# Kernel optimization log

Measured on AMD Instinct MI355X. Metric: run time of the kernel, lower is better.

Reference implementation:

```python
import jax, jax.numpy as jnp
import numpy as np

POOLED = 7          # output_size (7x7 bins)
SPATIAL_SCALE = 0.0625  # 1/16 backbone stride


def setup_inputs() -> dict:
    key = jax.random.key(0)
    k1, k2, k3, k4 = jax.random.split(key, 4)
    B, C, H, W = 4, 1029, 80, 80   # C = output_dim(21) * 7 * 7
    N = 1024                        # number of ROIs
    x = jax.random.normal(k1, (B, C, H, W), dtype=jnp.float32)
    img_w = W / SPATIAL_SCALE       # 1280 px
    img_h = H / SPATIAL_SCALE
    bidx = jax.random.randint(k2, (N,), 0, B).astype(jnp.float32)
    xs = jax.random.uniform(k3, (N, 2), dtype=jnp.float32) * img_w
    ys = jax.random.uniform(k4, (N, 2), dtype=jnp.float32) * img_h
    x1 = jnp.min(xs, axis=1); x2 = jnp.max(xs, axis=1)
    y1 = jnp.min(ys, axis=1); y2 = jnp.max(ys, axis=1)
    rois = jnp.stack([bidx, x1, y1, x2, y2], axis=1)  # [N,5]
    return {"input": x, "rois": rois}


def reference(input, rois):
    # Position-sensitive ROI average pooling (R-FCN / Caffe semantics).
    B, C, H, W = input.shape
    Ph = Pw = POOLED
    D = C // (Ph * Pw)  # output_dim
    N = rois.shape[0]

    # Summed-area table so each bin average is 4 gathers (same math as
    # summing the bin then dividing by its area). Padded with a zero row/col.
    sat = jnp.cumsum(jnp.cumsum(input, axis=2), axis=3)
    sat = jnp.pad(sat, ((0, 0), (0, 0), (1, 0), (1, 0)))

    b = rois[:, 0].astype(jnp.int32)
    rnd = lambda v: jnp.floor(v + 0.5)  # C round() for non-negative coords
    roi_sw = rnd(rois[:, 1]) * SPATIAL_SCALE
    roi_sh = rnd(rois[:, 2]) * SPATIAL_SCALE
    roi_ew = rnd(rois[:, 3] + 1.0) * SPATIAL_SCALE
    roi_eh = rnd(rois[:, 4] + 1.0) * SPATIAL_SCALE
    roi_w = jnp.maximum(roi_ew - roi_sw, 0.1)
    roi_h = jnp.maximum(roi_eh - roi_sh, 0.1)
    bin_h = roi_h / Ph  # [N]
    bin_w = roi_w / Pw

    ph = jnp.arange(Ph, dtype=jnp.float32)
    pw = jnp.arange(Pw, dtype=jnp.float32)
    hs = jnp.clip(jnp.floor(ph[None, :] * bin_h[:, None] + roi_sh[:, None]), 0, H).astype(jnp.int32)   # [N,Ph]
    he = jnp.clip(jnp.ceil((ph[None, :] + 1.0) * bin_h[:, None] + roi_sh[:, None]), 0, H).astype(jnp.int32)
    ws = jnp.clip(jnp.floor(pw[None, :] * bin_w[:, None] + roi_sw[:, None]), 0, W).astype(jnp.int32)   # [N,Pw]
    we = jnp.clip(jnp.ceil((pw[None, :] + 1.0) * bin_w[:, None] + roi_sw[:, None]), 0, W).astype(jnp.int32)

    # position-sensitive channel: c = (d*Ph + ph)*Pw + pw  -> [D,Ph,Pw]
    c = (jnp.arange(D)[:, None, None] * Ph + jnp.arange(Ph)[None, :, None]) * Pw + jnp.arange(Pw)[None, None, :]

    bI = b[:, None, None, None]          # [N,1,1,1]
    cI = c[None, :, :, :]                # [1,D,Ph,Pw]
    hsI = hs[:, None, :, None]; heI = he[:, None, :, None]  # [N,1,Ph,1]
    wsI = ws[:, None, None, :]; weI = we[:, None, None, :]  # [N,1,1,Pw]

    s = (sat[bI, cI, heI, weI] - sat[bI, cI, hsI, weI]
         - sat[bI, cI, heI, wsI] + sat[bI, cI, hsI, wsI])   # [N,D,Ph,Pw]

    area = ((he - hs)[:, None, :, None] * (we - ws)[:, None, None, :]).astype(input.dtype)
    out = jnp.where(area > 0, s / jnp.maximum(area, 1.0), jnp.zeros((), input.dtype))
    return out  # [N, D, Ph, Pw]
```

## Files before the change

### kernel.cpp

```cpp
#include <hip/hip_runtime.h>
#include <stdint.h>


#define PSB 4
#define PSC 1029
#define PSH 80
#define PSW 80
#define PSCALE 0.0625f
#define PLANE_ELEMS (PSH * PSW)
#define NMAX 1024

typedef __attribute__((address_space(3))) void lds_void;
typedef __attribute__((address_space(1))) void glob_void;

__global__ __launch_bounds__(256) void psroi_fused(
    const float* __restrict__ x,
    const float* __restrict__ rois,
    float* __restrict__ out,
    int N)
{
    const int blk = blockIdx.x;
    const int b   = blk / PSC;
    const int c   = blk - b * PSC;
    const int ph  = (c / 7) % 7;
    const int pw  = c % 7;

    __shared__ float    plane[PLANE_ELEMS];
    __shared__ uint32_t geomL[NMAX];
    __shared__ uint16_t nL[NMAX];

    const int tid  = threadIdx.x;
    const int lane = tid & 63;
    const int wv   = tid >> 6;

    {
        const float4* src4 = (const float4*)(x + ((size_t)b * PSC + c) * PLANE_ELEMS);
        float4* dst4 = (float4*)plane;
        #pragma unroll
        for (int i = 0; i < 6; ++i) {
            __builtin_amdgcn_global_load_lds(
                (const glob_void*)(src4 + tid + i * 256),
                (lds_void*)(dst4 + tid + i * 256), 16, 0, 0);
        }
        if (tid < 64) {
            __builtin_amdgcn_global_load_lds(
                (const glob_void*)(src4 + tid + 1536),
                (lds_void*)(dst4 + tid + 1536), 16, 0, 0);
        }
    }

    const float fph = (float)ph, fpw = (float)pw;
    int segCnt = 0;
    const int rounds = (N + 255) >> 8;
    for (int j = 0; j < rounds; ++j) {
        int n = j * 256 + wv * 64 + lane;
        bool match = false;
        uint32_t pack = 0;
        if (n < N) {
            const float* r = rois + (size_t)n * 5;
            float rb = r[0], r1 = r[1], r2 = r[2], r3 = r[3], r4 = r[4];
            match = ((int)rb == b);

            float roi_sw = floorf(r1 + 0.5f) * PSCALE;
            float roi_sh = floorf(r2 + 0.5f) * PSCALE;
            float roi_ew = floorf(r3 + 1.5f) * PSCALE;
            float roi_eh = floorf(r4 + 1.5f) * PSCALE;

            float bin_h = fmaxf(roi_eh - roi_sh, 0.1f) * (1.0f / 7.0f);
            float bin_w = fmaxf(roi_ew - roi_sw, 0.1f) * (1.0f / 7.0f);

            int hs = (int)fminf(fmaxf(floorf(fph * bin_h + roi_sh), 0.0f), (float)PSH);
            int he = (int)fminf(fmaxf(ceilf((fph + 1.0f) * bin_h + roi_sh), 0.0f), (float)PSH);
            int ws = (int)fminf(fmaxf(floorf(fpw * bin_w + roi_sw), 0.0f), (float)PSW);
            int we = (int)fminf(fmaxf(ceilf((fpw + 1.0f) * bin_w + roi_sw), 0.0f), (float)PSW);
            pack = (uint32_t)hs | ((uint32_t)he << 8) |
                   ((uint32_t)ws << 16) | ((uint32_t)we << 24);
        }
        unsigned long long mask = __ballot(match);
        int myoff = __popcll(mask & ((1ull << lane) - 1ull));
        if (match) {
            int s = wv * 256 + segCnt + myoff;
            geomL[s] = pack;
            nL[s]    = (uint16_t)n;
        }
        segCnt += (int)__popcll(mask);
    }

    __syncthreads();

    const float4* __restrict__ p4 = (const float4*)plane;

    for (int i = lane; i < segCnt; i += 64) {
        uint32_t g = geomL[wv * 256 + i];
        int n  = nL[wv * 256 + i];
        int hs = g & 0xFF, he = (g >> 8) & 0xFF;
        int ws = (g >> 16) & 0xFF, we = g >> 24;

        int a0   = ws >> 2;
        int nch  = (we > ws) ? (((we - 1) >> 2) - a0 + 1) : 0;
        int base = a0 * 4;

        float4 m0, m1, m2, m3;
        {
            int k;
            k = base;      m0.x = (k>=ws && k<we); k++; m0.y = (k>=ws && k<we); k++;
                           m0.z = (k>=ws && k<we); k++; m0.w = (k>=ws && k<we);
            k = base + 4;  m1.x = (k>=ws && k<we); k++; m1.y = (k>=ws && k<we); k++;
                           m1.z = (k>=ws && k<we); k++; m1.w = (k>=ws && k<we);
            k = base + 8;  m2.x = (k>=ws && k<we); k++; m2.y = (k>=ws && k<we); k++;
                           m2.z = (k>=ws && k<we); k++; m2.w = (k>=ws && k<we);
            k = base + 12; m3.x = (k>=ws && k<we); k++; m3.y = (k>=ws && k<we); k++;
                           m3.z = (k>=ws && k<we); k++; m3.w = (k>=ws && k<we);
        }

        float s = 0.0f;
        for (int h = hs; h < he; ++h) {
            const float4* rw = p4 + h * (PSW / 4) + a0;
            {
                float4 v = rw[0];
                s = fmaf(v.x, m0.x, s); s = fmaf(v.y, m0.y, s);
                s = fmaf(v.z, m0.z, s); s = fmaf(v.w, m0.w, s);
            }
            if (nch > 1) {
                float4 v = rw[1];
                s = fmaf(v.x, m1.x, s); s = fmaf(v.y, m1.y, s);
                s = fmaf(v.z, m1.z, s); s = fmaf(v.w, m1.w, s);
            }
            if (nch > 2) {
                float4 v = rw[2];
                s = fmaf(v.x, m2.x, s); s = fmaf(v.y, m2.y, s);
                s = fmaf(v.z, m2.z, s); s = fmaf(v.w, m2.w, s);
            }
            if (nch > 3) {
                float4 v = rw[3];
                s = fmaf(v.x, m3.x, s); s = fmaf(v.y, m3.y, s);
                s = fmaf(v.z, m3.z, s); s = fmaf(v.w, m3.w, s);
            }
        }

        int area = (he - hs) * (we - ws);
        out[(size_t)n * PSC + c] = (area > 0) ? s / (float)area : 0.0f;
    }
}

extern "C" void kernel_launch(void* const* d_in, const int* in_sizes, int n_in,
                              void* d_out, int out_size, void* d_ws, size_t ws_size,
                              hipStream_t stream) {
    const float* x    = (const float*)d_in[0];
    const float* rois = (const float*)d_in[1];
    float* out        = (float*)d_out;
    int N = in_sizes[1] / 5;

    psroi_fused<<<PSB * PSC, 256, 0, stream>>>(x, rois, out, N);
}
```

Measured before the change: 170.0 us.

## Process three channel planes per block with double-buffered async LDS staging

Each block now handles three channels that share the same (ph,pw) bin, so the ROI filtering, geometry, masks and reciprocal area are computed once and reused across all three planes. The planes are staged into two LDS buffers with global_load_lds, and manual vmcnt waits and barriers let the next plane load while the current one is summed. The grid shrinks to a third of its size and each block uses about twice the LDS, which lowers occupancy. The code hardcodes N=1024 (the ROI loads have no bounds check), and each wave now copies its own slice of the plane.

Result: no change. 173.3 us (+1.9%).

```diff
diff --git a/kernel.cpp b/kernel.cpp
--- a/kernel.cpp
+++ b/kernel.cpp
@@ -7,25 +7,95 @@
 #define PSH 80
 #define PSW 80
 #define PSCALE 0.0625f
-#define PLANE_ELEMS (PSH * PSW)
+#define PLANE_F4 1600
 #define NMAX 1024
+#define DCHUNK 3
+#define NCHUNK 7
 
 typedef __attribute__((address_space(3))) void lds_void;
 typedef __attribute__((address_space(1))) void glob_void;
 
-__global__ __launch_bounds__(256) void psroi_fused(
+#define VM_WAIT7() asm volatile("s_waitcnt vmcnt(7)" ::: "memory")
+#define VM_WAIT0() asm volatile("s_waitcnt vmcnt(0)" ::: "memory")
+#define BARRIER()  __builtin_amdgcn_s_barrier()
+#define SFENCE()   __builtin_amdgcn_sched_barrier(0)
+
+__device__ __forceinline__ void stage_plane(const float4* __restrict__ src4,
+                                            float4* dst4, int wv, int lane)
+{
+    const int base = wv * 400;
+    #pragma unroll
+    for (int i = 0; i < 6; ++i) {
+        int idx = base + i * 64 + lane;
+        __builtin_amdgcn_global_load_lds((const glob_void*)(src4 + idx),
+                                         (lds_void*)(dst4 + idx), 16, 0, 0);
+    }
+    int idx = base + 384 + lane;
+    if (lane < 16)
+        __builtin_amdgcn_global_load_lds((const glob_void*)(src4 + idx),
+                                         (lds_void*)(dst4 + idx), 16, 0, 0);
+}
+
+__device__ __forceinline__ void make_masks(int ws, int we, int base,
+                                           float4& m0, float4& m1,
+                                           float4& m2, float4& m3)
+{
+#define MK(K) (((K) >= ws && (K) < we) ? 1.0f : 0.0f)
+    m0 = make_float4(MK(base+0),  MK(base+1),  MK(base+2),  MK(base+3));
+    m1 = make_float4(MK(base+4),  MK(base+5),  MK(base+6),  MK(base+7));
+    m2 = make_float4(MK(base+8),  MK(base+9),  MK(base+10), MK(base+11));
+    m3 = make_float4(MK(base+12), MK(base+13), MK(base+14), MK(base+15));
+#undef MK
+}
+
+__device__ __forceinline__ float sum_roi(const float4* p4, int hs, int he,
+                                         int a0, int nch,
+                                         const float4& m0, const float4& m1,
+                                         const float4& m2, const float4& m3)
+{
+    float s = 0.0f;
+    for (int h = hs; h < he; ++h) {
+        const float4* rw = p4 + h * (PSW / 4) + a0;
+        float4 v = rw[0];
+        s = fmaf(v.x, m0.x, s); s = fmaf(v.y, m0.y, s);
+        s = fmaf(v.z, m0.z, s); s = fmaf(v.w, m0.w, s);
+        if (nch > 1) {
+            v = rw[1];
+            s = fmaf(v.x, m1.x, s); s = fmaf(v.y, m1.y, s);
+            s = fmaf(v.z, m1.z, s); s = fmaf(v.w, m1.w, s);
+        }
+        if (nch > 2) {
+            v = rw[2];
+            s = fmaf(v.x, m2.x, s); s = fmaf(v.y, m2.y, s);
+            s = fmaf(v.z, m2.z, s); s = fmaf(v.w, m2.w, s);
+        }
+        if (nch > 3) {
+            v = rw[3];
+            s = fmaf(v.x, m3.x, s); s = fmaf(v.y, m3.y, s);
+            s = fmaf(v.z, m3.z, s); s = fmaf(v.w, m3.w, s);
+        }
+    }
+    return s;
+}
+
+__global__ __launch_bounds__(256) void psroi_pipe(
     const float* __restrict__ x,
     const float* __restrict__ rois,
     float* __restrict__ out,
     int N)
 {
-    const int blk = blockIdx.x;
-    const int b   = blk / PSC;
-    const int c   = blk - b * PSC;
-    const int ph  = (c / 7) % 7;
-    const int pw  = c % 7;
-
-    __shared__ float    plane[PLANE_ELEMS];
+    const int blk   = blockIdx.x;
+    const int chunk = blk % NCHUNK;
+    const int t     = blk / NCHUNK;
+    const int pp    = t % 49;
+    const int b     = t / 49;
+    const int ph    = pp / 7;
+    const int pw    = pp % 7;
+    const int d0    = chunk * DCHUNK;
+    const int cb    = ph * 7 + pw;
+
+    __shared__ float4   bufA[PLANE_F4];
+    __shared__ float4   bufB[PLANE_F4];
     __shared__ uint32_t geomL[NMAX];
     __shared__ uint16_t nL[NMAX];
 
@@ -33,114 +103,127 @@
     const int lane = tid & 63;
     const int wv   = tid >> 6;
 
-    {
-        const float4* src4 = (const float4*)(x + ((size_t)b * PSC + c) * PLANE_ELEMS);
-        float4* dst4 = (float4*)plane;
-        #pragma unroll
-        for (int i = 0; i < 6; ++i) {
-            __builtin_amdgcn_global_load_lds(
-                (const glob_void*)(src4 + tid + i * 256),
-                (lds_void*)(dst4 + tid + i * 256), 16, 0, 0);
-        }
-        if (tid < 64) {
-            __builtin_amdgcn_global_load_lds(
-                (const glob_void*)(src4 + tid + 1536),
-                (lds_void*)(dst4 + tid + 1536), 16, 0, 0);
-        }
-    }
+    const float* xb = x + (size_t)b * PSC * (PSH * PSW);
+    const float4* src0 = (const float4*)(xb + (size_t)((d0 + 0) * 49 + cb) * (PSH * PSW));
+    const float4* src1 = (const float4*)(xb + (size_t)((d0 + 1) * 49 + cb) * (PSH * PSW));
+    const float4* src2 = (const float4*)(xb + (size_t)((d0 + 2) * 49 + cb) * (PSH * PSW));
+
+    float rb[4][5];
+    #pragma unroll
+    for (int j = 0; j < 4; ++j) {
+        const float* r = rois + (size_t)(j * 256 + wv * 64 + lane) * 5;
+        rb[j][0] = r[0]; rb[j][1] = r[1]; rb[j][2] = r[2];
+        rb[j][3] = r[3]; rb[j][4] = r[4];
+    }
+    SFENCE();
+
+    stage_plane(src0, bufA, wv, lane);
+    SFENCE();
 
     const float fph = (float)ph, fpw = (float)pw;
+    const int segBase = wv * 256;
     int segCnt = 0;
-    const int rounds = (N + 255) >> 8;
-    for (int j = 0; j < rounds; ++j) {
+    #pragma unroll
+    for (int j = 0; j < 4; ++j) {
         int n = j * 256 + wv * 64 + lane;
-        bool match = false;
-        uint32_t pack = 0;
-        if (n < N) {
-            const float* r = rois + (size_t)n * 5;
-            float rb = r[0], r1 = r[1], r2 = r[2], r3 = r[3], r4 = r[4];
-            match = ((int)rb == b);
-
-            float roi_sw = floorf(r1 + 0.5f) * PSCALE;
-            float roi_sh = floorf(r2 + 0.5f) * PSCALE;
-            float roi_ew = floorf(r3 + 1.5f) * PSCALE;
-            float roi_eh = floorf(r4 + 1.5f) * PSCALE;
-
-            float bin_h = fmaxf(roi_eh - roi_sh, 0.1f) * (1.0f / 7.0f);
-            float bin_w = fmaxf(roi_ew - roi_sw, 0.1f) * (1.0f / 7.0f);
-
-            int hs = (int)fminf(fmaxf(floorf(fph * bin_h + roi_sh), 0.0f), (float)PSH);
-            int he = (int)fminf(fmaxf(ceilf((fph + 1.0f) * bin_h + roi_sh), 0.0f), (float)PSH);
-            int ws = (int)fminf(fmaxf(floorf(fpw * bin_w + roi_sw), 0.0f), (float)PSW);
-            int we = (int)fminf(fmaxf(ceilf((fpw + 1.0f) * bin_w + roi_sw), 0.0f), (float)PSW);
-            pack = (uint32_t)hs | ((uint32_t)he << 8) |
-                   ((uint32_t)ws << 16) | ((uint32_t)we << 24);
-        }
+        bool match = ((int)rb[j][0] == b);
+
+        float roi_sw = floorf(rb[j][1] + 0.5f) * PSCALE;
+        float roi_sh = floorf(rb[j][2] + 0.5f) * PSCALE;
+        float roi_ew = floorf(rb[j][3] + 1.5f) * PSCALE;
+        float roi_eh = floorf(rb[j][4] + 1.5f) * PSCALE;
+
+        float bin_h = fmaxf(roi_eh - roi_sh, 0.1f) * (1.0f / 7.0f);
+        float bin_w = fmaxf(roi_ew - roi_sw, 0.1f) * (1.0f / 7.0f);
+
+        int hs = (int)fminf(fmaxf(floorf(fph * bin_h + roi_sh), 0.0f), (float)PSH);
+        int he = (int)fminf(fmaxf(ceilf((fph + 1.0f) * bin_h + roi_sh), 0.0f), (float)PSH);
+        int ws = (int)fminf(fmaxf(floorf(fpw * bin_w + roi_sw), 0.0f), (float)PSW);
+        int we = (int)fminf(fmaxf(ceilf((fpw + 1.0f) * bin_w + roi_sw), 0.0f), (float)PSW);
+
+        uint32_t pack = (uint32_t)hs | ((uint32_t)he << 8) |
+                        ((uint32_t)ws << 16) | ((uint32_t)we << 24);
+
         unsigned long long mask = __ballot(match);
-        int myoff = __popcll(mask & ((1ull << lane) - 1ull));
+        int off = __popcll(mask & ((1ull << lane) - 1ull));
         if (match) {
-            int s = wv * 256 + segCnt + myoff;
+            int s = segBase + segCnt + off;
             geomL[s] = pack;
             nL[s]    = (uint16_t)n;
         }
         segCnt += (int)__popcll(mask);
     }
 
-    __syncthreads();
-
-    const float4* __restrict__ p4 = (const float4*)plane;
-
-    for (int i = lane; i < segCnt; i += 64) {
-        uint32_t g = geomL[wv * 256 + i];
-        int n  = nL[wv * 256 + i];
-        int hs = g & 0xFF, he = (g >> 8) & 0xFF;
+    const bool has0 = lane < segCnt;
+    const bool has1 = (64 + lane) < segCnt;
+
+    int hs0=0, he0=0, a00=0, nch0=0, n0=0, area0=0;
+    float inv0 = 0.0f; float4 m00, m01, m02, m03;
+    m00 = m01 = m02 = m03 = make_float4(0, 0, 0, 0);
+    if (has0) {
+        uint32_t g = geomL[segBase + lane];
+        n0 = nL[segBase + lane];
+        hs0 = g & 0xFF; he0 = (g >> 8) & 0xFF;
         int ws = (g >> 16) & 0xFF, we = g >> 24;
-
-        int a0   = ws >> 2;
-        int nch  = (we > ws) ? (((we - 1) >> 2) - a0 + 1) : 0;
-        int base = a0 * 4;
-
-        float4 m0, m1, m2, m3;
-        {
-            int k;
-            k = base;      m0.x = (k>=ws && k<we); k++; m0.y = (k>=ws && k<we); k++;
-                           m0.z = (k>=ws && k<we); k++; m0.w = (k>=ws && k<we);
-            k = base + 4;  m1.x = (k>=ws && k<we); k++; m1.y = (k>=ws && k<we); k++;
-                           m1.z = (k>=ws && k<we); k++; m1.w = (k>=ws && k<we);
-            k = base + 8;  m2.x = (k>=ws && k<we); k++; m2.y = (k>=ws && k<we); k++;
-                           m2.z = (k>=ws && k<we); k++; m2.w = (k>=ws && k<we);
-            k = base + 12; m3.x = (k>=ws && k<we); k++; m3.y = (k>=ws && k<we); k++;
-                           m3.z = (k>=ws && k<we); k++; m3.w = (k>=ws && k<we);
-        }
-
-        float s = 0.0f;
-        for (int h = hs; h < he; ++h) {
-            const float4* rw = p4 + h * (PSW / 4) + a0;
-            {
-                float4 v = rw[0];
-                s = fmaf(v.x, m0.x, s); s = fmaf(v.y, m0.y, s);
-                s = fmaf(v.z, m0.z, s); s = fmaf(v.w, m0.w, s);
-            }
-            if (nch > 1) {
-                float4 v = rw[1];
-                s = fmaf(v.x, m1.x, s); s = fmaf(v.y, m1.y, s);
-                s = fmaf(v.z, m1.z, s); s = fmaf(v.w, m1.w, s);
-            }
-            if (nch > 2) {
-                float4 v = rw[2];
-                s = fmaf(v.x, m2.x, s); s = fmaf(v.y, m2.y, s);
-                s = fmaf(v.z, m2.z, s); s = fmaf(v.w, m2.w, s);
-            }
-            if (nch > 3) {
-                float4 v = rw[3];
-                s = fmaf(v.x, m3.x, s); s = fmaf(v.y, m3.y, s);
-                s = fmaf(v.z, m3.z, s); s = fmaf(v.w, m3.w, s);
-            }
-        }
-
-        int area = (he - hs) * (we - ws);
-        out[(size_t)n * PSC + c] = (area > 0) ? s / (float)area : 0.0f;
-    }
+        a00 = ws >> 2;
+        nch0 = (we > ws) ? (((we - 1) >> 2) - a00 + 1) : 0;
+        make_masks(ws, we, a00 * 4, m00, m01, m02, m03);
+        area0 = (he0 - hs0) * (we - ws);
+        inv0 = 1.0f / (float)(area0 > 0 ? area0 : 1);
+    }
+    int hs1=0, he1=0, a10=0, nch1=0, n1=0, area1=0;
+    float inv1 = 0.0f; float4 m10, m11, m12, m13;
+    m10 = m11 = m12 = m13 = make_float4(0, 0, 0, 0);
+    if (has1) {
+        uint32_t g = geomL[segBase + 64 + lane];
+        n1 = nL[segBase + 64 + lane];
+        hs1 = g & 0xFF; he1 = (g >> 8) & 0xFF;
+        int ws = (g >> 16) & 0xFF, we = g >> 24;
+        a10 = ws >> 2;
+        nch1 = (we > ws) ? (((we - 1) >> 2) - a10 + 1) : 0;
+        make_masks(ws, we, a10 * 4, m10, m11, m12, m13);
+        area1 = (he1 - hs1) * (we - ws);
+        inv1 = 1.0f / (float)(area1 > 0 ? area1 : 1);
+    }
+
+    auto sum_plane = [&](const float4* p4, int c) {
+        if (has0) {
+            float s = sum_roi(p4, hs0, he0, a00, nch0, m00, m01, m02, m03);
+            out[(size_t)n0 * PSC + c] = (area0 > 0) ? s * inv0 : 0.0f;
+        }
+        if (has1) {
+            float s = sum_roi(p4, hs1, he1, a10, nch1, m10, m11, m12, m13);
+            out[(size_t)n1 * PSC + c] = (area1 > 0) ? s * inv1 : 0.0f;
+        }
+        for (int i = 128 + lane; i < segCnt; i += 64) {
+            uint32_t g = geomL[segBase + i];
+            int n  = nL[segBase + i];
+            int hs = g & 0xFF, he = (g >> 8) & 0xFF;
+            int ws = (g >> 16) & 0xFF, we = g >> 24;
+            int a0 = ws >> 2;
+            int nch = (we > ws) ? (((we - 1) >> 2) - a0 + 1) : 0;
+            float4 q0, q1, q2, q3;
+            make_masks(ws, we, a0 * 4, q0, q1, q2, q3);
+            float s = sum_roi(p4, hs, he, a0, nch, q0, q1, q2, q3);
+            int area = (he - hs) * (we - ws);
+            out[(size_t)n * PSC + c] = (area > 0) ? s / (float)area : 0.0f;
+        }
+    };
+
+    stage_plane(src1, bufB, wv, lane);
+    VM_WAIT7();
+    BARRIER(); SFENCE();
+    sum_plane((const float4*)bufA, (d0 + 0) * 49 + cb);
+
+    BARRIER(); SFENCE();
+    stage_plane(src2, bufA, wv, lane);
+    VM_WAIT7();
+    BARRIER(); SFENCE();
+    sum_plane((const float4*)bufB, (d0 + 1) * 49 + cb);
+
+    VM_WAIT0();
+    BARRIER(); SFENCE();
+    sum_plane((const float4*)bufA, (d0 + 2) * 49 + cb);
 }
 
 extern "C" void kernel_launch(void* const* d_in, const int* in_sizes, int n_in,
@@ -151,5 +234,5 @@
     float* out        = (float*)d_out;
     int N = in_sizes[1] / 5;
 
-    psroi_fused<<<PSB * PSC, 256, 0, stream>>>(x, rois, out, N);
-}
+    psroi_pipe<<<PSB * 49 * NCHUNK, 256, 0, stream>>>(x, rois, out, N);
+}
```
